# Optimization experiments

Hardware: AMD Instinct MI355X
Metric: run time of the kernel (lower is better)

The kernel has to match this reference:

```python
import jax, jax.numpy as jnp
import numpy as np

N = 50000   # nodes
E = 500000  # edges
DIN = 128
DOUT = 128
H = 8       # mulhead
DH = DOUT // H
L = 2       # layers per branch
NC = 7      # emotion classes
EPS = 1e-9  # BatchNorm eps from source


def _bn(x):
    # BatchNorm1d in train mode, gamma=1/beta=0 at init
    m = x.mean(axis=0)
    v = x.var(axis=0)
    return (x - m) * jax.lax.rsqrt(v + EPS)


def _gat_forward(f, row, col, vals, Ws, bs, Wn, bn, As, An):
    for i in range(L):
        hs = jax.nn.relu(jnp.einsum('nd,hdk->nhk', f, Ws[i]) + bs[i])  # [N,H,DH]
        hn = jax.nn.relu(jnp.einsum('nd,hdk->nhk', f, Wn[i]) + bn[i])  # [N,H,DH]
        ats = jax.nn.leaky_relu(jnp.einsum('nhk,hk->nh', hs, As[i]), negative_slope=0.2)  # [N,H]
        # NOTE: source computes attention_neigh from f_self (faithful)
        atn = jax.nn.leaky_relu(jnp.einsum('nhk,hk->nh', hs, An[i]), negative_slope=0.2)  # [N,H]
        e = (ats[row] + atn[col]) * vals[:, None]            # [E,H] per-edge attention
        msg = e[:, :, None] * hn[col]                        # [E,H,DH] gather + weight
        agg = jax.ops.segment_sum(msg, row, num_segments=N)  # [N,H,DH] scatter-add (sparse mm)
        f = _bn(agg.reshape(N, H * DH))                      # concat heads + norm
    return f


def _gcn_forward(f, row, col, vals, W, b):
    for i in range(L):
        h = f @ W[i] + b[i]                                  # [N,DOUT]
        agg = jax.ops.segment_sum(vals[:, None] * h[col], row, num_segments=N)
        f = _bn(jax.nn.relu(agg))
    return f


def setup_inputs() -> dict:
    key = jax.random.key(0)
    ks = jax.random.split(key, 24)
    inp = {}
    inp['f_in'] = jax.random.normal(ks[0], (N, DIN), jnp.float32)
    inp['edge_row'] = jax.random.randint(ks[1], (E,), 0, N, jnp.int32)
    inp['edge_col'] = jax.random.randint(ks[2], (E,), 0, N, jnp.int32)
    inp['vals_gat'] = jax.random.uniform(ks[3], (E,), jnp.float32)
    inp['vals_uttr'] = jax.random.uniform(ks[4], (E,), jnp.float32)
    inp['vals_past'] = jax.random.uniform(ks[5], (E,), jnp.float32)
    inp['vals_futr'] = jax.random.uniform(ks[6], (E,), jnp.float32)
    s = 0.05
    # GAT params (stacked over [layer, head]); layer0 in=DIN, later in=DOUT (equal here)
    inp['gat_Ws'] = jax.random.normal(ks[7], (L, H, DIN, DH), jnp.float32) * s
    inp['gat_bs'] = jnp.zeros((L, H, DH), jnp.float32)
    inp['gat_Wn'] = jax.random.normal(ks[8], (L, H, DIN, DH), jnp.float32) * s
    inp['gat_bn'] = jnp.zeros((L, H, DH), jnp.float32)
    inp['gat_as'] = jnp.ones((L, H, DH), jnp.float32)  # init ones per source
    inp['gat_an'] = jnp.ones((L, H, DH), jnp.float32)
    # three vanilla GCN branches
    inp['W_uttr'] = jax.random.normal(ks[9], (L, DIN, DOUT), jnp.float32) * s
    inp['b_uttr'] = jnp.zeros((L, DOUT), jnp.float32)
    inp['W_past'] = jax.random.normal(ks[10], (L, DIN, DOUT), jnp.float32) * s
    inp['b_past'] = jnp.zeros((L, DOUT), jnp.float32)
    inp['W_futr'] = jax.random.normal(ks[11], (L, DIN, DOUT), jnp.float32) * s
    inp['b_futr'] = jnp.zeros((L, DOUT), jnp.float32)
    # self perceptron + classifier
    inp['W_self'] = jax.random.normal(ks[12], (DIN, DOUT), jnp.float32) * s
    inp['b_self'] = jnp.zeros((DOUT,), jnp.float32)
    inp['W_cls'] = jax.random.normal(ks[13], (5 * DOUT, NC), jnp.float32) * s
    inp['b_cls'] = jnp.zeros((NC,), jnp.float32)
    return inp


def reference(f_in, edge_row, edge_col, vals_gat, vals_uttr, vals_past, vals_futr,
              gat_Ws, gat_bs, gat_Wn, gat_bn, gat_as, gat_an,
              W_uttr, b_uttr, W_past, b_past, W_futr, b_futr,
              W_self, b_self, W_cls, b_cls):
    o_gat = _gat_forward(f_in, edge_row, edge_col, vals_gat,
                         gat_Ws, gat_bs, gat_Wn, gat_bn, gat_as, gat_an)
    o_uttr = _gcn_forward(f_in, edge_row, edge_col, vals_uttr, W_uttr, b_uttr)
    o_past = _gcn_forward(f_in, edge_row, edge_col, vals_past, W_past, b_past)
    o_futr = _gcn_forward(f_in, edge_row, edge_col, vals_futr, W_futr, b_futr)
    o_self = _bn(jax.nn.relu(f_in @ W_self + b_self))
    f = jnp.concatenate([o_gat, o_uttr, o_past, o_futr, o_self], axis=1)  # [N,640]
    return f @ W_cls + b_cls  # classifier: act=False, plain linear
```

## Files before the change

kernel.cpp:

```cpp
#include <hip/hip_runtime.h>
#include <hip/hip_bf16.h>


#define NN 50000
#define NE 500000
#define DD 128
#define NH 8
#define DHD 16
#define NCLS 7
#define SCAN_B 196

typedef __attribute__((ext_vector_type(8))) short short8;
typedef __attribute__((ext_vector_type(4))) float f32x4;

__device__ __forceinline__ unsigned short f2bf(float x) {
    unsigned int u = __float_as_uint(x);
    unsigned int r = (u + 0x7fffu + ((u >> 16) & 1u)) >> 16;
    return (unsigned short)r;
}
__device__ __forceinline__ unsigned int pack2bf(float lo, float hi) {
    return (unsigned int)f2bf(lo) | ((unsigned int)f2bf(hi) << 16);
}
__device__ __forceinline__ float bflo(unsigned int u) { return __uint_as_float(u << 16); }
__device__ __forceinline__ float bfhi(unsigned int u) { return __uint_as_float(u & 0xffff0000u); }


__global__ void count_kernel(const int* __restrict__ row, int* __restrict__ cnt) {
    int e = blockIdx.x * 256 + threadIdx.x;
    if (e < NE) atomicAdd(&cnt[row[e]], 1);
}

__global__ __launch_bounds__(256) void scan1_kernel(const int* __restrict__ cnt,
                                                    int* __restrict__ pre,
                                                    int* __restrict__ bsum) {
    __shared__ int s[256];
    int t = threadIdx.x;
    int i = blockIdx.x * 256 + t;
    int v = (i < NN) ? cnt[i] : 0;
    s[t] = v;
    __syncthreads();
    for (int off = 1; off < 256; off <<= 1) {
        int u = (t >= off) ? s[t - off] : 0;
        __syncthreads();
        s[t] += u;
        __syncthreads();
    }
    if (i < NN) pre[i] = s[t] - v;
    if (t == 255) bsum[blockIdx.x] = s[255];
}

__global__ __launch_bounds__(256) void scan2_kernel(const int* __restrict__ bsum,
                                                    int* __restrict__ boff) {
    __shared__ int s[256];
    int t = threadIdx.x;
    int v = (t < SCAN_B) ? bsum[t] : 0;
    s[t] = v;
    __syncthreads();
    for (int off = 1; off < 256; off <<= 1) {
        int u = (t >= off) ? s[t - off] : 0;
        __syncthreads();
        s[t] += u;
        __syncthreads();
    }
    boff[t] = s[t] - v;
    if (t == 255) boff[256] = s[255];
}

__global__ __launch_bounds__(256) void scan3_kernel(const int* __restrict__ pre,
                                                    const int* __restrict__ boff,
                                                    int* __restrict__ row_ptr,
                                                    int* __restrict__ fill) {
    int t = threadIdx.x;
    int i = blockIdx.x * 256 + t;
    if (i < NN) {
        int v = pre[i] + boff[blockIdx.x];
        row_ptr[i] = v;
        fill[i] = v;
    }
    if (blockIdx.x == 0 && t == 0) row_ptr[NN] = boff[256];
}

__global__ void scatter_kernel(const int* __restrict__ row, const int* __restrict__ col,
                               const float* __restrict__ vg, const float* __restrict__ vu,
                               const float* __restrict__ vp, const float* __restrict__ vf,
                               int* __restrict__ fill, int4* __restrict__ ed) {
    int e = blockIdx.x * 256 + threadIdx.x;
    if (e >= NE) return;
    int r = row[e];
    int pos = atomicAdd(&fill[r], 1);
    ed[2 * pos] = make_int4(col[e], __float_as_int(vg[e]), __float_as_int(vu[e]),
                            __float_as_int(vp[e]));
    ed[2 * pos + 1] = make_int4(__float_as_int(vf[e]), 0, 0, 0);
}


__global__ __launch_bounds__(256) void tobf16_kernel(const float* __restrict__ x,
                                                     short* __restrict__ y) {
    int idx = blockIdx.x * 256 + threadIdx.x;
    if (idx >= NN * DD / 8) return;
    float4 a = ((const float4*)x)[idx * 2];
    float4 b = ((const float4*)x)[idx * 2 + 1];
    uint4 o;
    o.x = pack2bf(a.x, a.y);
    o.y = pack2bf(a.z, a.w);
    o.z = pack2bf(b.x, b.y);
    o.w = pack2bf(b.z, b.w);
    *(uint4*)(y + (size_t)idx * 8) = o;
}


struct WPrepArgs {
    const float* src[11];
};

__global__ __launch_bounds__(256) void wprep_kernel(WPrepArgs a, short* __restrict__ out) {
    int idx = blockIdx.x * 256 + threadIdx.x;
    if (idx >= 11 * DD * DD) return;
    int w = idx >> 14;
    int r = idx & 16383;
    int n = r >> 7, k = r & 127;
    const float* W = a.src[w];
    float v = (w < 4) ? W[(size_t)((n >> 4) * DD + k) * DHD + (n & 15)] : W[(size_t)k * DD + n];
    out[idx] = (short)f2bf(v);
}


struct WFixArgs {
    const float* W1[3];
    const float* b1[3];
    const float* stats[3];
};

__global__ __launch_bounds__(256) void wfix_kernel(WFixArgs a, short* __restrict__ wt_out,
                                                   float* __restrict__ bfix) {
    int idx = blockIdx.x * 256 + threadIdx.x;
    if (idx >= 3 * DD) return;
    int br = idx >> 7, n = idx & 127;
    const float* st = a.stats[br];
    const float* W = a.W1[br];
    const float inv_n = 1.0f / (float)NN;
    float accb = 0.f;
    short* wo = wt_out + (size_t)br * DD * DD + (size_t)n * DD;
#pragma unroll 4
    for (int k = 0; k < DD; ++k) {
        float m = st[k] * inv_n;
        float var = st[DD + k] * inv_n - m * m;
        float s = rsqrtf(var + 1e-9f);
        float w = W[(size_t)k * DD + n];
        wo[k] = (short)f2bf(s * w);
        accb += m * s * w;
    }
    bfix[idx] = a.b1[br][n] - accb;
}


__global__ __launch_bounds__(256) void mfma_mm_self(const short* __restrict__ A,
                                                    const short* __restrict__ Wt,
                                                    const float* __restrict__ bias,
                                                    float* __restrict__ stats_out,
                                                    float* __restrict__ C) {
    __shared__ short As[64 * DD];
    int t = threadIdx.x;
    int r0 = blockIdx.x * 64;
    {
        int srow = t >> 2;
        int sk0 = (t & 3) * 32;
        int grow = r0 + srow;
#pragma unroll
        for (int j = 0; j < 4; ++j) {
            int k0 = sk0 + j * 8;
            short8 frag = {0, 0, 0, 0, 0, 0, 0, 0};
            if (grow < NN) frag = *(const short8*)(A + (size_t)grow * DD + k0);
            int byte = srow * 256 + k0 * 2;
            byte ^= (srow & 7) << 4;
            *(short8*)((char*)As + byte) = frag;
        }
    }
    __syncthreads();
    int w = t >> 6, l = t & 63;
    int c0 = w * 32;
    int lr = l & 15, lg = l >> 4;
    f32x4 acc[4][2] = {};
#pragma unroll
    for (int s = 0; s < 4; ++s) {
        short8 af[4];
#pragma unroll
        for (int f = 0; f < 4; ++f) {
            int rr = f * 16 + lr;
            int byte = rr * 256 + (s * 32 + lg * 8) * 2;
            byte ^= (rr & 7) << 4;
            af[f] = *(const short8*)((const char*)As + byte);
        }
#pragma unroll
        for (int g = 0; g < 2; ++g) {
            int col = c0 + g * 16 + lr;
            short8 bf = *(const short8*)&Wt[(size_t)col * DD + s * 32 + lg * 8];
#pragma unroll
            for (int f = 0; f < 4; ++f)
                acc[f][g] = __builtin_amdgcn_mfma_f32_16x16x32_bf16(af[f], bf, acc[f][g], 0, 0, 0);
        }
    }
    float sA[2] = {0.f, 0.f}, qA[2] = {0.f, 0.f};
#pragma unroll
    for (int g = 0; g < 2; ++g) {
        int col = c0 + g * 16 + lr;
        float b = bias[col];
#pragma unroll
        for (int f = 0; f < 4; ++f)
#pragma unroll
            for (int i = 0; i < 4; ++i) {
                int row = r0 + f * 16 + lg * 4 + i;
                if (row < NN) {
                    float o = fmaxf(acc[f][g][i] + b, 0.f);
                    C[(size_t)row * DD + col] = o;
                    sA[g] += o;
                    qA[g] += o * o;
                }
            }
    }
#pragma unroll
    for (int g = 0; g < 2; ++g) {
        sA[g] += __shfl_xor(sA[g], 16);
        sA[g] += __shfl_xor(sA[g], 32);
        qA[g] += __shfl_xor(qA[g], 16);
        qA[g] += __shfl_xor(qA[g], 32);
    }
    if (lg == 0)
#pragma unroll
        for (int g = 0; g < 2; ++g) {
            int col = c0 + g * 16 + lr;
            atomicAdd(&stats_out[col], sA[g]);
            atomicAdd(&stats_out[DD + col], qA[g]);
        }
}


struct MMB {
    const short* A[3];
    const short* W[3];
    const float* bias[3];
    const float* rs[3];
    float* stats[3];
    short* C[3];
};

__global__ __launch_bounds__(256) void mfma_mm_gcn(MMB m) {
    int br = blockIdx.y;
    const short* A = m.A[br];
    const short* Wt = m.W[br];
    const float* bias = m.bias[br];
    const float* rs = m.rs[br];
    float* stats_out = m.stats[br];
    short* C = m.C[br];

    __shared__ short As[64 * DD];
    int t = threadIdx.x;
    int r0 = blockIdx.x * 64;
    {
        int srow = t >> 2;
        int sk0 = (t & 3) * 32;
        int grow = r0 + srow;
#pragma unroll
        for (int j = 0; j < 4; ++j) {
            int k0 = sk0 + j * 8;
            short8 frag = {0, 0, 0, 0, 0, 0, 0, 0};
            if (grow < NN) frag = *(const short8*)(A + (size_t)grow * DD + k0);
            int byte = srow * 256 + k0 * 2;
            byte ^= (srow & 7) << 4;
            *(short8*)((char*)As + byte) = frag;
        }
    }
    __syncthreads();
    int w = t >> 6, l = t & 63;
    int c0 = w * 32;
    int lr = l & 15, lg = l >> 4;
    f32x4 acc[4][2] = {};
#pragma unroll
    for (int s = 0; s < 4; ++s) {
        short8 af[4];
#pragma unroll
        for (int f = 0; f < 4; ++f) {
            int rr = f * 16 + lr;
            int byte = rr * 256 + (s * 32 + lg * 8) * 2;
            byte ^= (rr & 7) << 4;
            af[f] = *(const short8*)((const char*)As + byte);
        }
#pragma unroll
        for (int g = 0; g < 2; ++g) {
            int col = c0 + g * 16 + lr;
            short8 bf = *(const short8*)&Wt[(size_t)col * DD + s * 32 + lg * 8];
#pragma unroll
            for (int f = 0; f < 4; ++f)
                acc[f][g] = __builtin_amdgcn_mfma_f32_16x16x32_bf16(af[f], bf, acc[f][g], 0, 0, 0);
        }
    }
    float rsv[4][4];
#pragma unroll
    for (int f = 0; f < 4; ++f)
#pragma unroll
        for (int i = 0; i < 4; ++i) {
            int row = r0 + f * 16 + lg * 4 + i;
            rsv[f][i] = (row < NN) ? rs[row] : 0.f;
        }
    float sA[2] = {0.f, 0.f}, qA[2] = {0.f, 0.f};
#pragma unroll
    for (int g = 0; g < 2; ++g) {
        int col = c0 + g * 16 + lr;
        float b = bias[col];
#pragma unroll
        for (int f = 0; f < 4; ++f)
#pragma unroll
            for (int i = 0; i < 4; ++i) {
                int row = r0 + f * 16 + lg * 4 + i;
                if (row < NN) {
                    float o = fmaxf(acc[f][g][i] + rsv[f][i] * b, 0.f);
                    C[(size_t)row * DD + col] = (short)f2bf(o);
                    sA[g] += o;
                    qA[g] += o * o;
                }
            }
    }
#pragma unroll
    for (int g = 0; g < 2; ++g) {
        sA[g] += __shfl_xor(sA[g], 16);
        sA[g] += __shfl_xor(sA[g], 32);
        qA[g] += __shfl_xor(qA[g], 16);
        qA[g] += __shfl_xor(qA[g], 32);
    }
    if (lg == 0)
#pragma unroll
        for (int g = 0; g < 2; ++g) {
            int col = c0 + g * 16 + lr;
            atomicAdd(&stats_out[col], sA[g]);
            atomicAdd(&stats_out[DD + col], qA[g]);
        }
}


template <int PRE>
__global__ __launch_bounds__(256) void mfma_mm_pair(const void* __restrict__ Av,
                                                    const short* __restrict__ Wt1,
                                                    const short* __restrict__ Wt2,
                                                    const float* __restrict__ b1,
                                                    const float* __restrict__ b2,
                                                    const float* __restrict__ a_se,
                                                    const float* __restrict__ a_ne,
                                                    const float* __restrict__ stats_in,
                                                    short* __restrict__ out2,
                                                    float* __restrict__ ats_o,
                                                    float* __restrict__ atn_o) {
    __shared__ short As[64 * DD];
    __shared__ float mS[DD], sS[DD];
    int t = threadIdx.x;
    int r0 = blockIdx.x * 64;
    if (PRE == 1) {
        if (t < DD) {
            const float inv_n = 1.0f / (float)NN;
            float m = stats_in[t] * inv_n;
            float var = stats_in[DD + t] * inv_n - m * m;
            mS[t] = m;
            sS[t] = rsqrtf(var + 1e-9f);
        }
        __syncthreads();
    }
    {
        int srow = t >> 2;
        int sk0 = (t & 3) * 32;
        int grow = r0 + srow;
#pragma unroll
        for (int j = 0; j < 4; ++j) {
            int k0 = sk0 + j * 8;
            short8 frag = {0, 0, 0, 0, 0, 0, 0, 0};
            if (grow < NN) {
                if (PRE == 0) {
                    frag = *(const short8*)((const short*)Av + (size_t)grow * DD + k0);
                } else {
                    const float* Ar = (const float*)Av + (size_t)grow * DD;
                    float4 v0 = *(const float4*)(Ar + k0);
                    float4 v1 = *(const float4*)(Ar + k0 + 4);
                    float vv[8] = {v0.x, v0.y, v0.z, v0.w, v1.x, v1.y, v1.z, v1.w};
#pragma unroll
                    for (int e = 0; e < 8; ++e)
                        frag[e] = (short)f2bf((vv[e] - mS[k0 + e]) * sS[k0 + e]);
                }
            }
            int byte = srow * 256 + k0 * 2;
            byte ^= (srow & 7) << 4;
            *(short8*)((char*)As + byte) = frag;
        }
    }
    __syncthreads();
    int w = t >> 6, l = t & 63;
    int c0 = w * 32;
    int lr = l & 15, lg = l >> 4;
    f32x4 acc1[4][2] = {}, acc2[4][2] = {};
#pragma unroll
    for (int s = 0; s < 4; ++s) {
        short8 af[4];
#pragma unroll
        for (int f = 0; f < 4; ++f) {
            int rr = f * 16 + lr;
            int byte = rr * 256 + (s * 32 + lg * 8) * 2;
            byte ^= (rr & 7) << 4;
            af[f] = *(const short8*)((const char*)As + byte);
        }
#pragma unroll
        for (int g = 0; g < 2; ++g) {
            int col = c0 + g * 16 + lr;
            short8 bfa = *(const short8*)&Wt1[(size_t)col * DD + s * 32 + lg * 8];
            short8 bfb = *(const short8*)&Wt2[(size_t)col * DD + s * 32 + lg * 8];
#pragma unroll
            for (int f = 0; f < 4; ++f) {
                acc1[f][g] = __builtin_amdgcn_mfma_f32_16x16x32_bf16(af[f], bfa, acc1[f][g], 0, 0, 0);
                acc2[f][g] = __builtin_amdgcn_mfma_f32_16x16x32_bf16(af[f], bfb, acc2[f][g], 0, 0, 0);
            }
        }
    }
#pragma unroll
    for (int g = 0; g < 2; ++g) {
        int colc = c0 + g * 16 + lr;
        float bb1 = b1[colc], bb2 = b2[colc];
        float asv = a_se[colc], anv = a_ne[colc];
        int h = (c0 >> 4) + g;
#pragma unroll
        for (int f = 0; f < 4; ++f)
#pragma unroll
            for (int i = 0; i < 4; ++i) {
                int row = r0 + f * 16 + lg * 4 + i;
                float o1 = fmaxf(acc1[f][g][i] + bb1, 0.f);
                float o2 = fmaxf(acc2[f][g][i] + bb2, 0.f);
                if (row < NN) out2[(size_t)row * DD + colc] = (short)f2bf(o2);
                float ds = o1 * asv, dn = o1 * anv;
                ds += __shfl_xor(ds, 1);
                dn += __shfl_xor(dn, 1);
                ds += __shfl_xor(ds, 2);
                dn += __shfl_xor(dn, 2);
                ds += __shfl_xor(ds, 4);
                dn += __shfl_xor(dn, 4);
                ds += __shfl_xor(ds, 8);
                dn += __shfl_xor(dn, 8);
                if (lr == 0 && row < NN) {
                    ats_o[row * NH + h] = ds > 0.f ? ds : 0.2f * ds;
                    atn_o[row * NH + h] = dn > 0.f ? dn : 0.2f * dn;
                }
            }
    }
}


__global__ __launch_bounds__(256) void spmm_fusedA(
    const short* __restrict__ hnb, const short* __restrict__ fbf, const float* __restrict__ ats,
    const float* __restrict__ atn, const int4* __restrict__ ed, const int* __restrict__ row_ptr,
    float* __restrict__ aggG, short* __restrict__ zu, short* __restrict__ zp,
    short* __restrict__ zf, float* __restrict__ rs_all) {
    int r = __builtin_amdgcn_readfirstlane((blockIdx.x * 256 + threadIdx.x) >> 6);
    int lane = threadIdx.x & 63;
    if (r >= NN) return;
    int hh = lane >> 3;
    float a_s = ats[r * NH + hh];
    int start = row_ptr[r], end = row_ptr[r + 1];
    float2 ag = {0.f, 0.f}, au = {0.f, 0.f}, ap = {0.f, 0.f}, af2 = {0.f, 0.f};
    float su = 0.f, sp = 0.f, sf = 0.f;
    int j = start;
    for (; j + 2 <= end; j += 2) {
        int4 a0 = ed[2 * j], b0 = ed[2 * j + 1];
        int4 a1 = ed[2 * j + 2], b1 = ed[2 * j + 3];
        int cA = a0.x, cB = a1.x;
        float at0 = atn[cA * NH + hh], at1 = atn[cB * NH + hh];
        unsigned int g0 = *(const unsigned int*)(hnb + (size_t)cA * DD + lane * 2);
        unsigned int f0 = *(const unsigned int*)(fbf + (size_t)cA * DD + lane * 2);
        unsigned int g1 = *(const unsigned int*)(hnb + (size_t)cB * DD + lane * 2);
        unsigned int f1 = *(const unsigned int*)(fbf + (size_t)cB * DD + lane * 2);
        {
            float vg = __int_as_float(a0.y), vu = __int_as_float(a0.z);
            float vp = __int_as_float(a0.w), vf = __int_as_float(b0.x);
            float e = (a_s + at0) * vg;
            float glo = bflo(g0), ghi = bfhi(g0), flo = bflo(f0), fhi = bfhi(f0);
            ag.x += e * glo;  ag.y += e * ghi;
            au.x += vu * flo; au.y += vu * fhi;
            ap.x += vp * flo; ap.y += vp * fhi;
            af2.x += vf * flo; af2.y += vf * fhi;
            su += vu; sp += vp; sf += vf;
        }
        {
            float vg = __int_as_float(a1.y), vu = __int_as_float(a1.z);
            float vp = __int_as_float(a1.w), vf = __int_as_float(b1.x);
            float e = (a_s + at1) * vg;
            float glo = bflo(g1), ghi = bfhi(g1), flo = bflo(f1), fhi = bfhi(f1);
            ag.x += e * glo;  ag.y += e * ghi;
            au.x += vu * flo; au.y += vu * fhi;
            ap.x += vp * flo; ap.y += vp * fhi;
            af2.x += vf * flo; af2.y += vf * fhi;
            su += vu; sp += vp; sf += vf;
        }
    }
    if (j < end) {
        int4 a0 = ed[2 * j], b0 = ed[2 * j + 1];
        int cA = a0.x;
        float at0 = atn[cA * NH + hh];
        unsigned int g0 = *(const unsigned int*)(hnb + (size_t)cA * DD + lane * 2);
        unsigned int f0 = *(const unsigned int*)(fbf + (size_t)cA * DD + lane * 2);
        float vg = __int_as_float(a0.y), vu = __int_as_float(a0.z);
        float vp = __int_as_float(a0.w), vf = __int_as_float(b0.x);
        float e = (a_s + at0) * vg;
        float glo = bflo(g0), ghi = bfhi(g0), flo = bflo(f0), fhi = bfhi(f0);
        ag.x += e * glo;  ag.y += e * ghi;
        au.x += vu * flo; au.y += vu * fhi;
        ap.x += vp * flo; ap.y += vp * fhi;
        af2.x += vf * flo; af2.y += vf * fhi;
        su += vu; sp += vp; sf += vf;
    }
    size_t o = (size_t)r * DD + lane * 2;
    *(float2*)&aggG[o] = ag;
    *(unsigned int*)(zu + o) = pack2bf(au.x, au.y);
    *(unsigned int*)(zp + o) = pack2bf(ap.x, ap.y);
    *(unsigned int*)(zf + o) = pack2bf(af2.x, af2.y);
    if (lane == 0) {
        rs_all[r] = su;
        rs_all[NN + r] = sp;
        rs_all[2 * NN + r] = sf;
    }
}


__global__ __launch_bounds__(256) void spmm_fusedB(
    const short* __restrict__ hnb, const short* __restrict__ y0u, const short* __restrict__ y0p,
    const short* __restrict__ y0f, const float* __restrict__ ats, const float* __restrict__ atn,
    const int4* __restrict__ ed, const int* __restrict__ row_ptr, float* __restrict__ aggG,
    short* __restrict__ z1u, short* __restrict__ z1p, short* __restrict__ z1f) {
    int r = __builtin_amdgcn_readfirstlane((blockIdx.x * 256 + threadIdx.x) >> 6);
    int lane = threadIdx.x & 63;
    if (r >= NN) return;
    int hh = lane >> 3;
    float a_s = ats[r * NH + hh];
    int start = row_ptr[r], end = row_ptr[r + 1];
    float2 ag = {0.f, 0.f}, au = {0.f, 0.f}, ap = {0.f, 0.f}, af2 = {0.f, 0.f};
    int j = start;
    for (; j + 2 <= end; j += 2) {
        int4 a0 = ed[2 * j], b0 = ed[2 * j + 1];
        int4 a1 = ed[2 * j + 2], b1 = ed[2 * j + 3];
        int cA = a0.x, cB = a1.x;
        float at0 = atn[cA * NH + hh], at1 = atn[cB * NH + hh];
        size_t oA = (size_t)cA * DD + lane * 2, oB = (size_t)cB * DD + lane * 2;
        unsigned int g0 = *(const unsigned int*)(hnb + oA);
        unsigned int u0 = *(const unsigned int*)(y0u + oA);
        unsigned int p0 = *(const unsigned int*)(y0p + oA);
        unsigned int q0 = *(const unsigned int*)(y0f + oA);
        unsigned int g1 = *(const unsigned int*)(hnb + oB);
        unsigned int u1 = *(const unsigned int*)(y0u + oB);
        unsigned int p1 = *(const unsigned int*)(y0p + oB);
        unsigned int q1 = *(const unsigned int*)(y0f + oB);
        float e0 = (a_s + at0) * __int_as_float(a0.y);
        float e1 = (a_s + at1) * __int_as_float(a1.y);
        float vu0 = __int_as_float(a0.z), vp0 = __int_as_float(a0.w), vf0 = __int_as_float(b0.x);
        float vu1 = __int_as_float(a1.z), vp1 = __int_as_float(a1.w), vf1 = __int_as_float(b1.x);
        ag.x += e0 * bflo(g0) + e1 * bflo(g1);
        ag.y += e0 * bfhi(g0) + e1 * bfhi(g1);
        au.x += vu0 * bflo(u0) + vu1 * bflo(u1);
        au.y += vu0 * bfhi(u0) + vu1 * bfhi(u1);
        ap.x += vp0 * bflo(p0) + vp1 * bflo(p1);
        ap.y += vp0 * bfhi(p0) + vp1 * bfhi(p1);
        af2.x += vf0 * bflo(q0) + vf1 * bflo(q1);
        af2.y += vf0 * bfhi(q0) + vf1 * bfhi(q1);
    }
    if (j < end) {
        int4 a0 = ed[2 * j], b0 = ed[2 * j + 1];
        int cA = a0.x;
        float at0 = atn[cA * NH + hh];
        size_t oA = (size_t)cA * DD + lane * 2;
        unsigned int g0 = *(const unsigned int*)(hnb + oA);
        unsigned int u0 = *(const unsigned int*)(y0u + oA);
        unsigned int p0 = *(const unsigned int*)(y0p + oA);
        unsigned int q0 = *(const unsigned int*)(y0f + oA);
        float e0 = (a_s + at0) * __int_as_float(a0.y);
        float vu0 = __int_as_float(a0.z), vp0 = __int_as_float(a0.w), vf0 = __int_as_float(b0.x);
        ag.x += e0 * bflo(g0);
        ag.y += e0 * bfhi(g0);
        au.x += vu0 * bflo(u0);
        au.y += vu0 * bfhi(u0);
        ap.x += vp0 * bflo(p0);
        ap.y += vp0 * bfhi(p0);
        af2.x += vf0 * bflo(q0);
        af2.y += vf0 * bfhi(q0);
    }
    size_t o = (size_t)r * DD + lane * 2;
    *(float2*)&aggG[o] = ag;
    *(unsigned int*)(z1u + o) = pack2bf(au.x, au.y);
    *(unsigned int*)(z1p + o) = pack2bf(ap.x, ap.y);
    *(unsigned int*)(z1f + o) = pack2bf(af2.x, af2.y);
}


__global__ __launch_bounds__(256) void bn_stats_kernel(const float* __restrict__ x,
                                                       float* __restrict__ stats) {
    int c = threadIdx.x & 127;
    int sub = threadIdx.x >> 7;
    int rows_per_block = (NN + gridDim.x - 1) / gridDim.x;
    int rbeg = blockIdx.x * rows_per_block;
    int rend = min(rbeg + rows_per_block, NN);
    float s = 0.f, q = 0.f;
    for (int r = rbeg + sub; r < rend; r += 2) {
        float v = x[(size_t)r * DD + c];
        s += v;
        q += v * v;
    }
    atomicAdd(&stats[c], s);
    atomicAdd(&stats[DD + c], q);
}


template <int PRE, bool FIRST, bool BF16IN>
__global__ __launch_bounds__(256) void cls_acc_kernel(const void* __restrict__ ov,
                                                      const float* __restrict__ Wc,
                                                      const float* __restrict__ stats,
                                                      const float* __restrict__ b_cls,
                                                      float* __restrict__ out) {
    __shared__ float Wl[DD * NCLS];
    __shared__ float mS[DD], sS[DD];
    int t = threadIdx.x;
    for (int i = t; i < DD * NCLS; i += 256) Wl[i] = Wc[i];
    if (PRE && t < DD) {
        const float inv_n = 1.0f / (float)NN;
        float m = stats[t] * inv_n;
        float var = stats[DD + t] * inv_n - m * m;
        mS[t] = m;
        sS[t] = rsqrtf(var + 1e-9f);
    }
    __syncthreads();
    int n = blockIdx.x * 256 + t;
    if (n >= NN) return;
    float acc[NCLS] = {};
    if (BF16IN) {
        const uint4* orow = (const uint4*)((const short*)ov + (size_t)n * DD);
        for (int k8 = 0; k8 < DD / 8; ++k8) {
            uint4 v = orow[k8];
            float vv[8] = {bflo(v.x), bfhi(v.x), bflo(v.y), bfhi(v.y),
                           bflo(v.z), bfhi(v.z), bflo(v.w), bfhi(v.w)};
#pragma unroll
            for (int kk = 0; kk < 8; ++kk) {
                int k = k8 * 8 + kk;
                float a = vv[kk];
                if (PRE == 2) a = fmaxf(a, 0.f);
                if (PRE) a = (a - mS[k]) * sS[k];
#pragma unroll
                for (int c = 0; c < NCLS; ++c) acc[c] += a * Wl[k * NCLS + c];
            }
        }
    } else {
        const float4* orow = (const float4*)((const float*)ov + (size_t)n * DD);
        for (int k4 = 0; k4 < DD / 4; ++k4) {
            float4 v = orow[k4];
#pragma unroll
            for (int kk = 0; kk < 4; ++kk) {
                int k = k4 * 4 + kk;
                float a = ((const float*)&v)[kk];
                if (PRE == 2) a = fmaxf(a, 0.f);
                if (PRE) a = (a - mS[k]) * sS[k];
#pragma unroll
                for (int c = 0; c < NCLS; ++c) acc[c] += a * Wl[k * NCLS + c];
            }
        }
    }
#pragma unroll
    for (int c = 0; c < NCLS; ++c) {
        if (FIRST)
            out[n * NCLS + c] = acc[c] + b_cls[c];
        else
            out[n * NCLS + c] += acc[c];
    }
}


extern "C" void kernel_launch(void* const* d_in, const int* in_sizes, int n_in, void* d_out,
                              int out_size, void* d_ws, size_t ws_size, hipStream_t stream) {
    const float* f_in = (const float*)d_in[0];
    const int* edge_row = (const int*)d_in[1];
    const int* edge_col = (const int*)d_in[2];
    const float* vals_gat = (const float*)d_in[3];
    const float* vals_uttr = (const float*)d_in[4];
    const float* vals_past = (const float*)d_in[5];
    const float* vals_futr = (const float*)d_in[6];
    const float* gat_Ws = (const float*)d_in[7];
    const float* gat_bs = (const float*)d_in[8];
    const float* gat_Wn = (const float*)d_in[9];
    const float* gat_bn = (const float*)d_in[10];
    const float* gat_as = (const float*)d_in[11];
    const float* gat_an = (const float*)d_in[12];
    const float* W_uttr = (const float*)d_in[13];
    const float* b_uttr = (const float*)d_in[14];
    const float* W_past = (const float*)d_in[15];
    const float* b_past = (const float*)d_in[16];
    const float* W_futr = (const float*)d_in[17];
    const float* b_futr = (const float*)d_in[18];
    const float* W_self = (const float*)d_in[19];
    const float* b_self = (const float*)d_in[20];
    const float* W_cls = (const float*)d_in[21];
    const float* b_cls = (const float*)d_in[22];
    float* out = (float*)d_out;

    char* ws = (char*)d_ws;
    size_t off = 0;
    auto alloc = [&](size_t bytes) -> void* {
        void* p = ws + off;
        off = (off + bytes + 255) & ~(size_t)255;
        return p;
    };
    float* stats_all = (float*)alloc(9 * 2 * DD * 4);
    int* cnt = (int*)alloc((size_t)NN * 4);
    float* tmp1 = (float*)alloc((size_t)NN * DD * 4);
    float* bufA = (float*)alloc((size_t)NN * DD * 4);
    short* fbf = (short*)alloc((size_t)NN * DD * 2);
    short* hnb = (short*)alloc((size_t)NN * DD * 2);
    short* z0u = (short*)alloc((size_t)NN * DD * 2);
    short* z0p = (short*)alloc((size_t)NN * DD * 2);
    short* z0f = (short*)alloc((size_t)NN * DD * 2);
    float* rs_all = (float*)alloc((size_t)3 * NN * 4);
    float* ats_b = (float*)alloc((size_t)NN * NH * 4);
    float* atn_b = (float*)alloc((size_t)NN * NH * 4);
    short* Wt_all = (short*)alloc((size_t)14 * DD * DD * 2);
    float* bfix = (float*)alloc((size_t)3 * DD * 4);
    int* row_ptr = (int*)alloc((size_t)(NN + 1) * 4);
    int* fill = (int*)alloc((size_t)NN * 4);
    int* pre_b = (int*)alloc((size_t)NN * 4);
    int* bsum = (int*)alloc((size_t)SCAN_B * 4);
    int* boff = (int*)alloc((size_t)257 * 4);
    int4* ed = (int4*)alloc((size_t)NE * 32);

    auto stats = [&](int s) { return stats_all + (size_t)s * 2 * DD; };
    auto Wt = [&](int w) { return Wt_all + (size_t)w * DD * DD; };

    const int gE = (NE + 255) / 256;
    const int gMM = (NN + 63) / 64;
    const int gSP = (NN + 3) / 4;
    const int gCA = (NN + 255) / 256;
    const int gBF = (NN * DD / 8 + 255) / 256;

    hipMemsetAsync(stats_all, 0, 9 * 2 * DD * 4 + (size_t)NN * 4, stream);

    count_kernel<<<gE, 256, 0, stream>>>(edge_row, cnt);
    scan1_kernel<<<SCAN_B, 256, 0, stream>>>(cnt, pre_b, bsum);
    scan2_kernel<<<1, 256, 0, stream>>>(bsum, boff);
    scan3_kernel<<<SCAN_B, 256, 0, stream>>>(pre_b, boff, row_ptr, fill);
    scatter_kernel<<<gE, 256, 0, stream>>>(edge_row, edge_col, vals_gat, vals_uttr, vals_past,
                                           vals_futr, fill, ed);

    tobf16_kernel<<<gBF, 256, 0, stream>>>(f_in, fbf);

    WPrepArgs wa;
    wa.src[0] = gat_Ws;
    wa.src[1] = gat_Wn;
    wa.src[2] = gat_Ws + (size_t)DD * DD;
    wa.src[3] = gat_Wn + (size_t)DD * DD;
    wa.src[4] = W_uttr;
    wa.src[5] = W_uttr + (size_t)DD * DD;
    wa.src[6] = W_past;
    wa.src[7] = W_past + (size_t)DD * DD;
    wa.src[8] = W_futr;
    wa.src[9] = W_futr + (size_t)DD * DD;
    wa.src[10] = W_self;
    wprep_kernel<<<(11 * DD * DD + 255) / 256, 256, 0, stream>>>(wa, Wt_all);

    mfma_mm_self<<<gMM, 256, 0, stream>>>(fbf, Wt(10), b_self, stats(8), tmp1);
    cls_acc_kernel<1, true, false><<<gCA, 256, 0, stream>>>(tmp1, W_cls + (size_t)4 * DD * NCLS,
                                                            stats(8), b_cls, out);

    mfma_mm_pair<0><<<gMM, 256, 0, stream>>>(fbf, Wt(0), Wt(1), gat_bs, gat_bn, gat_as, gat_an,
                                             nullptr, hnb, ats_b, atn_b);
    spmm_fusedA<<<gSP, 256, 0, stream>>>(hnb, fbf, ats_b, atn_b, ed, row_ptr, bufA, z0u, z0p,
                                         z0f, rs_all);
    bn_stats_kernel<<<256, 256, 0, stream>>>(bufA, stats(0));
    mfma_mm_pair<1><<<gMM, 256, 0, stream>>>(bufA, Wt(2), Wt(3), gat_bs + DD, gat_bn + DD,
                                             gat_as + DD, gat_an + DD, stats(0), hnb, ats_b,
                                             atn_b);

    const float* bb[3] = {b_uttr, b_past, b_futr};
    const float* Worig[3] = {W_uttr, W_past, W_futr};
    MMB m0;
    short* z0a[3] = {z0u, z0p, z0f};
    for (int br = 0; br < 3; ++br) {
        m0.A[br] = z0a[br];
        m0.W[br] = Wt(4 + br * 2);
        m0.bias[br] = bb[br];
        m0.rs[br] = rs_all + (size_t)br * NN;
        m0.stats[br] = stats(2 + br);
        m0.C[br] = z0a[br];
    }
    mfma_mm_gcn<<<dim3(gMM, 3), 256, 0, stream>>>(m0);

    WFixArgs wf;
    for (int br = 0; br < 3; ++br) {
        wf.W1[br] = Worig[br] + (size_t)DD * DD;
        wf.b1[br] = bb[br] + DD;
        wf.stats[br] = stats(2 + br);
    }
    wfix_kernel<<<2, 256, 0, stream>>>(wf, Wt(11), bfix);

    short* z1u = fbf;
    short* z1p = (short*)tmp1;
    short* z1f = (short*)tmp1 + (size_t)NN * DD;
    spmm_fusedB<<<gSP, 256, 0, stream>>>(hnb, z0u, z0p, z0f, ats_b, atn_b, ed, row_ptr, bufA,
                                         z1u, z1p, z1f);
    bn_stats_kernel<<<256, 256, 0, stream>>>(bufA, stats(1));
    cls_acc_kernel<1, false, false><<<gCA, 256, 0, stream>>>(bufA, W_cls, stats(1), b_cls, out);

    MMB m1;
    short* z1a[3] = {z1u, z1p, z1f};
    for (int br = 0; br < 3; ++br) {
        m1.A[br] = z1a[br];
        m1.W[br] = Wt(11 + br);
        m1.bias[br] = bfix + (size_t)br * DD;
        m1.rs[br] = rs_all + (size_t)br * NN;
        m1.stats[br] = stats(5 + br);
        m1.C[br] = z0a[br];
    }
    mfma_mm_gcn<<<dim3(gMM, 3), 256, 0, stream>>>(m1);

    for (int br = 0; br < 3; ++br)
        cls_acc_kernel<1, false, true><<<gCA, 256, 0, stream>>>(
            z0a[br], W_cls + (size_t)(DD + DD * br) * NCLS, stats(5 + br), b_cls, out);
}
```

Before: 572.8 us.

## Pack edge records to 16 bytes with bf16 values, merge classifier launches

Edge records drop from 32 to 16 bytes. The column index goes into the low 16 bits and the four edge weights are stored as bf16, which halves edge-stream traffic in both SpMM kernels. The column field is masked with 0xffff even though N=50000 fits, and the bf16 edge values lose precision. BN stats now use float4 loads with a shared-memory reduction, and the three GCN classifier launches become one 2D-grid kernel that accumulates with atomics.

Result: faster. 543.7 us (-5.1%).

```diff
diff --git a/kernel.cpp b/kernel.cpp
--- a/kernel.cpp
+++ b/kernel.cpp
@@ -88,9 +88,10 @@
     if (e >= NE) return;
     int r = row[e];
     int pos = atomicAdd(&fill[r], 1);
-    ed[2 * pos] = make_int4(col[e], __float_as_int(vg[e]), __float_as_int(vu[e]),
-                            __float_as_int(vp[e]));
-    ed[2 * pos + 1] = make_int4(__float_as_int(vf[e]), 0, 0, 0);
+    unsigned int x = (unsigned int)col[e] | ((unsigned int)f2bf(vg[e]) << 16);
+    unsigned int y = (unsigned int)f2bf(vu[e]) | ((unsigned int)f2bf(vp[e]) << 16);
+    unsigned int z = (unsigned int)f2bf(vf[e]);
+    ed[pos] = make_int4((int)x, (int)y, (int)z, 0);
 }
 
 
@@ -151,6 +152,42 @@
         accb += m * s * w;
     }
     bfix[idx] = a.b1[br][n] - accb;
+}
+
+
+__global__ __launch_bounds__(256) void bn_stats_kernel(const float* __restrict__ x,
+                                                       float* __restrict__ stats) {
+    __shared__ float sred[2 * DD];
+    int t = threadIdx.x;
+    sred[t] = 0.f;
+    __syncthreads();
+    int c4 = t & 31;
+    int sub = t >> 5;
+    int rows_per_block = (NN + gridDim.x - 1) / gridDim.x;
+    int rbeg = blockIdx.x * rows_per_block;
+    int rend = min(rbeg + rows_per_block, NN);
+    float s[4] = {}, q[4] = {};
+    for (int r = rbeg + sub; r < rend; r += 8) {
+        float4 v = *(const float4*)&x[(size_t)r * DD + c4 * 4];
+        s[0] += v.x; q[0] += v.x * v.x;
+        s[1] += v.y; q[1] += v.y * v.y;
+        s[2] += v.z; q[2] += v.z * v.z;
+        s[3] += v.w; q[3] += v.w * v.w;
+    }
+#pragma unroll
+    for (int i = 0; i < 4; ++i) {
+        s[i] += __shfl_xor(s[i], 32);
+        q[i] += __shfl_xor(q[i], 32);
+    }
+    if ((t & 32) == 0) {
+#pragma unroll
+        for (int i = 0; i < 4; ++i) {
+            atomicAdd(&sred[c4 * 4 + i], s[i]);
+            atomicAdd(&sred[DD + c4 * 4 + i], q[i]);
+        }
+    }
+    __syncthreads();
+    atomicAdd(&stats[t], sred[t]);
 }
 
 
@@ -463,17 +500,16 @@
     float su = 0.f, sp = 0.f, sf = 0.f;
     int j = start;
     for (; j + 2 <= end; j += 2) {
-        int4 a0 = ed[2 * j], b0 = ed[2 * j + 1];
-        int4 a1 = ed[2 * j + 2], b1 = ed[2 * j + 3];
-        int cA = a0.x, cB = a1.x;
+        int4 e0 = ed[j], e1 = ed[j + 1];
+        int cA = e0.x & 0xffff, cB = e1.x & 0xffff;
         float at0 = atn[cA * NH + hh], at1 = atn[cB * NH + hh];
         unsigned int g0 = *(const unsigned int*)(hnb + (size_t)cA * DD + lane * 2);
         unsigned int f0 = *(const unsigned int*)(fbf + (size_t)cA * DD + lane * 2);
         unsigned int g1 = *(const unsigned int*)(hnb + (size_t)cB * DD + lane * 2);
         unsigned int f1 = *(const unsigned int*)(fbf + (size_t)cB * DD + lane * 2);
         {
-            float vg = __int_as_float(a0.y), vu = __int_as_float(a0.z);
-            float vp = __int_as_float(a0.w), vf = __int_as_float(b0.x);
+            float vg = bfhi((unsigned)e0.x), vu = bflo((unsigned)e0.y);
+            float vp = bfhi((unsigned)e0.y), vf = bflo((unsigned)e0.z);
             float e = (a_s + at0) * vg;
             float glo = bflo(g0), ghi = bfhi(g0), flo = bflo(f0), fhi = bfhi(f0);
             ag.x += e * glo;  ag.y += e * ghi;
@@ -483,8 +519,8 @@
             su += vu; sp += vp; sf += vf;
         }
         {
-            float vg = __int_as_float(a1.y), vu = __int_as_float(a1.z);
-            float vp = __int_as_float(a1.w), vf = __int_as_float(b1.x);
+            float vg = bfhi((unsigned)e1.x), vu = bflo((unsigned)e1.y);
+            float vp = bfhi((unsigned)e1.y), vf = bflo((unsigned)e1.z);
             float e = (a_s + at1) * vg;
             float glo = bflo(g1), ghi = bfhi(g1), flo = bflo(f1), fhi = bfhi(f1);
             ag.x += e * glo;  ag.y += e * ghi;
@@ -495,13 +531,13 @@
         }
     }
     if (j < end) {
-        int4 a0 = ed[2 * j], b0 = ed[2 * j + 1];
-        int cA = a0.x;
+        int4 e0 = ed[j];
+        int cA = e0.x & 0xffff;
         float at0 = atn[cA * NH + hh];
         unsigned int g0 = *(const unsigned int*)(hnb + (size_t)cA * DD + lane * 2);
         unsigned int f0 = *(const unsigned int*)(fbf + (size_t)cA * DD + lane * 2);
-        float vg = __int_as_float(a0.y), vu = __int_as_float(a0.z);
-        float vp = __int_as_float(a0.w), vf = __int_as_float(b0.x);
+        float vg = bfhi((unsigned)e0.x), vu = bflo((unsigned)e0.y);
+        float vp = bfhi((unsigned)e0.y), vf = bflo((unsigned)e0.z);
         float e = (a_s + at0) * vg;
         float glo = bflo(g0), ghi = bfhi(g0), flo = bflo(f0), fhi = bfhi(f0);
         ag.x += e * glo;  ag.y += e * ghi;
@@ -537,9 +573,8 @@
     float2 ag = {0.f, 0.f}, au = {0.f, 0.f}, ap = {0.f, 0.f}, af2 = {0.f, 0.f};
     int j = start;
     for (; j + 2 <= end; j += 2) {
-        int4 a0 = ed[2 * j], b0 = ed[2 * j + 1];
-        int4 a1 = ed[2 * j + 2], b1 = ed[2 * j + 3];
-        int cA = a0.x, cB = a1.x;
+        int4 e0 = ed[j], e1 = ed[j + 1];
+        int cA = e0.x & 0xffff, cB = e1.x & 0xffff;
         float at0 = atn[cA * NH + hh], at1 = atn[cB * NH + hh];
         size_t oA = (size_t)cA * DD + lane * 2, oB = (size_t)cB * DD + lane * 2;
         unsigned int g0 = *(const unsigned int*)(hnb + oA);
@@ -550,12 +585,12 @@
         unsigned int u1 = *(const unsigned int*)(y0u + oB);
         unsigned int p1 = *(const unsigned int*)(y0p + oB);
         unsigned int q1 = *(const unsigned int*)(y0f + oB);
-        float e0 = (a_s + at0) * __int_as_float(a0.y);
-        float e1 = (a_s + at1) * __int_as_float(a1.y);
-        float vu0 = __int_as_float(a0.z), vp0 = __int_as_float(a0.w), vf0 = __int_as_float(b0.x);
-        float vu1 = __int_as_float(a1.z), vp1 = __int_as_float(a1.w), vf1 = __int_as_float(b1.x);
-        ag.x += e0 * bflo(g0) + e1 * bflo(g1);
-        ag.y += e0 * bfhi(g0) + e1 * bfhi(g1);
+        float ea0 = (a_s + at0) * bfhi((unsigned)e0.x);
+        float ea1 = (a_s + at1) * bfhi((unsigned)e1.x);
+        float vu0 = bflo((unsigned)e0.y), vp0 = bfhi((unsigned)e0.y), vf0 = bflo((unsigned)e0.z);
+        float vu1 = bflo((unsigned)e1.y), vp1 = bfhi((unsigned)e1.y), vf1 = bflo((unsigned)e1.z);
+        ag.x += ea0 * bflo(g0) + ea1 * bflo(g1);
+        ag.y += ea0 * bfhi(g0) + ea1 * bfhi(g1);
         au.x += vu0 * bflo(u0) + vu1 * bflo(u1);
         au.y += vu0 * bfhi(u0) + vu1 * bfhi(u1);
         ap.x += vp0 * bflo(p0) + vp1 * bflo(p1);
@@ -564,18 +599,18 @@
         af2.y += vf0 * bfhi(q0) + vf1 * bfhi(q1);
     }
     if (j < end) {
-        int4 a0 = ed[2 * j], b0 = ed[2 * j + 1];
-        int cA = a0.x;
+        int4 e0 = ed[j];
+        int cA = e0.x & 0xffff;
         float at0 = atn[cA * NH + hh];
         size_t oA = (size_t)cA * DD + lane * 2;
         unsigned int g0 = *(const unsigned int*)(hnb + oA);
         unsigned int u0 = *(const unsigned int*)(y0u + oA);
         unsigned int p0 = *(const unsigned int*)(y0p + oA);
         unsigned int q0 = *(const unsigned int*)(y0f + oA);
-        float e0 = (a_s + at0) * __int_as_float(a0.y);
-        float vu0 = __int_as_float(a0.z), vp0 = __int_as_float(a0.w), vf0 = __int_as_float(b0.x);
-        ag.x += e0 * bflo(g0);
-        ag.y += e0 * bfhi(g0);
+        float ea0 = (a_s + at0) * bfhi((unsigned)e0.x);
+        float vu0 = bflo((unsigned)e0.y), vp0 = bfhi((unsigned)e0.y), vf0 = bflo((unsigned)e0.z);
+        ag.x += ea0 * bflo(g0);
+        ag.y += ea0 * bfhi(g0);
         au.x += vu0 * bflo(u0);
         au.y += vu0 * bfhi(u0);
         ap.x += vp0 * bflo(p0);
@@ -591,26 +626,8 @@
 }
 
 
-__global__ __launch_bounds__(256) void bn_stats_kernel(const float* __restrict__ x,
-                                                       float* __restrict__ stats) {
-    int c = threadIdx.x & 127;
-    int sub = threadIdx.x >> 7;
-    int rows_per_block = (NN + gridDim.x - 1) / gridDim.x;
-    int rbeg = blockIdx.x * rows_per_block;
-    int rend = min(rbeg + rows_per_block, NN);
-    float s = 0.f, q = 0.f;
-    for (int r = rbeg + sub; r < rend; r += 2) {
-        float v = x[(size_t)r * DD + c];
-        s += v;
-        q += v * v;
-    }
-    atomicAdd(&stats[c], s);
-    atomicAdd(&stats[DD + c], q);
-}
-
-
-template <int PRE, bool FIRST, bool BF16IN>
-__global__ __launch_bounds__(256) void cls_acc_kernel(const void* __restrict__ ov,
+template <bool FIRST>
+__global__ __launch_bounds__(256) void cls_acc_kernel(const float* __restrict__ o,
                                                       const float* __restrict__ Wc,
                                                       const float* __restrict__ stats,
                                                       const float* __restrict__ b_cls,
@@ -619,7 +636,7 @@
     __shared__ float mS[DD], sS[DD];
     int t = threadIdx.x;
     for (int i = t; i < DD * NCLS; i += 256) Wl[i] = Wc[i];
-    if (PRE && t < DD) {
+    if (t < DD) {
         const float inv_n = 1.0f / (float)NN;
         float m = stats[t] * inv_n;
         float var = stats[DD + t] * inv_n - m * m;
@@ -630,35 +647,15 @@
     int n = blockIdx.x * 256 + t;
     if (n >= NN) return;
     float acc[NCLS] = {};
-    if (BF16IN) {
-        const uint4* orow = (const uint4*)((const short*)ov + (size_t)n * DD);
-        for (int k8 = 0; k8 < DD / 8; ++k8) {
-            uint4 v = orow[k8];
-            float vv[8] = {bflo(v.x), bfhi(v.x), bflo(v.y), bfhi(v.y),
-                           bflo(v.z), bfhi(v.z), bflo(v.w), bfhi(v.w)};
-#pragma unroll
-            for (int kk = 0; kk < 8; ++kk) {
-                int k = k8 * 8 + kk;
-                float a = vv[kk];
-                if (PRE == 2) a = fmaxf(a, 0.f);
-                if (PRE) a = (a - mS[k]) * sS[k];
-#pragma unroll
-                for (int c = 0; c < NCLS; ++c) acc[c] += a * Wl[k * NCLS + c];
-            }
-        }
-    } else {
-        const float4* orow = (const float4*)((const float*)ov + (size_t)n * DD);
-        for (int k4 = 0; k4 < DD / 4; ++k4) {
-            float4 v = orow[k4];
-#pragma unroll
-            for (int kk = 0; kk < 4; ++kk) {
-                int k = k4 * 4 + kk;
-                float a = ((const float*)&v)[kk];
-                if (PRE == 2) a = fmaxf(a, 0.f);
-                if (PRE) a = (a - mS[k]) * sS[k];
-#pragma unroll
-                for (int c = 0; c < NCLS; ++c) acc[c] += a * Wl[k * NCLS + c];
-            }
+    const float4* orow = (const float4*)(o + (size_t)n * DD);
+    for (int k4 = 0; k4 < DD / 4; ++k4) {
+        float4 v = orow[k4];
+#pragma unroll
+        for (int kk = 0; kk < 4; ++kk) {
+            int k = k4 * 4 + kk;
+            float a = (((const float*)&v)[kk] - mS[k]) * sS[k];
+#pragma unroll
+            for (int c = 0; c < NCLS; ++c) acc[c] += a * Wl[k * NCLS + c];
         }
     }
 #pragma unroll
@@ -668,6 +665,50 @@
         else
             out[n * NCLS + c] += acc[c];
     }
+}
+
+
+struct CLS3 {
+    const short* o[3];
+    const float* stats[3];
+};
+
+__global__ __launch_bounds__(256) void cls3_kernel(CLS3 a, const float* __restrict__ W_cls,
+                                                   float* __restrict__ out) {
+    int br = blockIdx.y;
+    const short* o = a.o[br];
+    const float* st = a.stats[br];
+    const float* Wc = W_cls + (size_t)(DD + DD * br) * NCLS;
+    __shared__ float Wl[DD * NCLS];
+    __shared__ float mS[DD], sS[DD];
+    int t = threadIdx.x;
+    for (int i = t; i < DD * NCLS; i += 256) Wl[i] = Wc[i];
+    if (t < DD) {
+        const float inv_n = 1.0f / (float)NN;
+        float m = st[t] * inv_n;
+        float var = st[DD + t] * inv_n - m * m;
+        mS[t] = m;
+        sS[t] = rsqrtf(var + 1e-9f);
+    }
+    __syncthreads();
+    int n = blockIdx.x * 256 + t;
+    if (n >= NN) return;
+    float acc[NCLS] = {};
+    const uint4* orow = (const uint4*)(o + (size_t)n * DD);
+    for (int k8 = 0; k8 < DD / 8; ++k8) {
+        uint4 v = orow[k8];
+        float vv[8] = {bflo(v.x), bfhi(v.x), bflo(v.y), bfhi(v.y),
+                       bflo(v.z), bfhi(v.z), bflo(v.w), bfhi(v.w)};
+#pragma unroll
+        for (int kk = 0; kk < 8; ++kk) {
+            int k = k8 * 8 + kk;
+            float a2 = (vv[kk] - mS[k]) * sS[k];
+#pragma unroll
+            for (int c = 0; c < NCLS; ++c) acc[c] += a2 * Wl[k * NCLS + c];
+        }
+    }
+#pragma unroll
+    for (int c = 0; c < NCLS; ++c) atomicAdd(&out[n * NCLS + c], acc[c]);
 }
 
 
@@ -724,14 +765,14 @@
     int* pre_b = (int*)alloc((size_t)NN * 4);
     int* bsum = (int*)alloc((size_t)SCAN_B * 4);
     int* boff = (int*)alloc((size_t)257 * 4);
-    int4* ed = (int4*)alloc((size_t)NE * 32);
+    int4* ed = (int4*)alloc((size_t)NE * 16);
 
     auto stats = [&](int s) { return stats_all + (size_t)s * 2 * DD; };
     auto Wt = [&](int w) { return Wt_all + (size_t)w * DD * DD; };
 
     const int gE = (NE + 255) / 256;
     const int gMM = (NN + 63) / 64;
-    const int gSP = (NN + 3) / 4;
+    const int gSP = NN / 4;
     const int gCA = (NN + 255) / 256;
     const int gBF = (NN * DD / 8 + 255) / 256;
 
@@ -761,14 +802,15 @@
     wprep_kernel<<<(11 * DD * DD + 255) / 256, 256, 0, stream>>>(wa, Wt_all);
 
     mfma_mm_self<<<gMM, 256, 0, stream>>>(fbf, Wt(10), b_self, stats(8), tmp1);
-    cls_acc_kernel<1, true, false><<<gCA, 256, 0, stream>>>(tmp1, W_cls + (size_t)4 * DD * NCLS,
-                                                            stats(8), b_cls, out);
+    cls_acc_kernel<true><<<gCA, 256, 0, stream>>>(tmp1, W_cls + (size_t)4 * DD * NCLS, stats(8),
+                                                  b_cls, out);
 
     mfma_mm_pair<0><<<gMM, 256, 0, stream>>>(fbf, Wt(0), Wt(1), gat_bs, gat_bn, gat_as, gat_an,
                                              nullptr, hnb, ats_b, atn_b);
     spmm_fusedA<<<gSP, 256, 0, stream>>>(hnb, fbf, ats_b, atn_b, ed, row_ptr, bufA, z0u, z0p,
                                          z0f, rs_all);
     bn_stats_kernel<<<256, 256, 0, stream>>>(bufA, stats(0));
+
     mfma_mm_pair<1><<<gMM, 256, 0, stream>>>(bufA, Wt(2), Wt(3), gat_bs + DD, gat_bn + DD,
                                              gat_as + DD, gat_an + DD, stats(0), hnb, ats_b,
                                              atn_b);
@@ -801,7 +843,7 @@
     spmm_fusedB<<<gSP, 256, 0, stream>>>(hnb, z0u, z0p, z0f, ats_b, atn_b, ed, row_ptr, bufA,
                                          z1u, z1p, z1f);
     bn_stats_kernel<<<256, 256, 0, stream>>>(bufA, stats(1));
-    cls_acc_kernel<1, false, false><<<gCA, 256, 0, stream>>>(bufA, W_cls, stats(1), b_cls, out);
+    cls_acc_kernel<false><<<gCA, 256, 0, stream>>>(bufA, W_cls, stats(1), b_cls, out);
 
     MMB m1;
     short* z1a[3] = {z1u, z1p, z1f};
@@ -815,7 +857,10 @@
     }
     mfma_mm_gcn<<<dim3(gMM, 3), 256, 0, stream>>>(m1);
 
-    for (int br = 0; br < 3; ++br)
-        cls_acc_kernel<1, false, true><<<gCA, 256, 0, stream>>>(
-            z0a[br], W_cls + (size_t)(DD + DD * br) * NCLS, stats(5 + br), b_cls, out);
-}
+    CLS3 c3;
+    for (int br = 0; br < 3; ++br) {
+        c3.o[br] = z0a[br];
+        c3.stats[br] = stats(5 + br);
+    }
+    cls3_kernel<<<dim3(gCA, 3), 256, 0, stream>>>(c3, W_cls, out);
+}
```
